# Kernel tuning notes

Hardware: AMD Instinct MI355X
Metric: run time of the kernel (lower is better)

## Reference

```python
import jax, jax.numpy as jnp
import numpy as np

N_NODES = 50000
IN_DIM = 256
LATENT = 128
HIDDEN = 2 * LATENT  # 256


def _xavier(key, fan_in, fan_out):
    # matches nn.init.xavier_uniform_ on a [out, in] weight; we store as [in, out]
    limit = float(np.sqrt(6.0 / (fan_in + fan_out)))
    return jax.random.uniform(key, (fan_in, fan_out), jnp.float32, -limit, limit)


def setup_inputs() -> dict:
    key = jax.random.key(0)
    ks = jax.random.split(key, 8)
    x = jax.random.normal(ks[0], (N_NODES, IN_DIM), jnp.float32)
    edge_index = jax.random.randint(ks[1], (2, 800000), 0, N_NODES, jnp.int64)
    W1 = _xavier(ks[2], IN_DIM, HIDDEN)
    b1 = jnp.zeros((HIDDEN,), jnp.float32)
    Wmu = _xavier(ks[3], HIDDEN, LATENT)
    bmu = jnp.zeros((LATENT,), jnp.float32)
    Wlv = _xavier(ks[4], HIDDEN, LATENT)
    blv = jnp.zeros((LATENT,), jnp.float32)
    return {"x": x, "edge_index": edge_index, "W1": W1, "b1": b1,
            "Wmu": Wmu, "bmu": bmu, "Wlv": Wlv, "blv": blv}


def _gcn_layer(x, W, b, src, dst):
    # PyG GCNConv: h = x @ W; add self loops; symmetric norm; scatter-add; + bias
    h = x @ W  # [N, out]
    ones = jnp.ones(src.shape[0], x.dtype)
    deg = jax.ops.segment_sum(ones, dst, num_segments=N_NODES) + 1.0  # +1 for self loop
    dinv = jax.lax.rsqrt(deg)  # deg >= 1 always
    norm = dinv[src] * dinv[dst]  # [E]
    agg = jax.ops.segment_sum(h[src] * norm[:, None], dst, num_segments=N_NODES)
    agg = agg + h * (dinv * dinv)[:, None]  # self-loop contribution, norm_ii = 1/deg_i
    return agg + b


def reference(x, edge_index, W1, b1, Wmu, bmu, Wlv, blv):
    src, dst = edge_index[0], edge_index[1]
    z = _gcn_layer(x, W1, b1, src, dst)
    z = jax.nn.relu(z)
    # dropout in eval mode == identity
    mu = _gcn_layer(z, Wmu, bmu, src, dst)
    logvar = _gcn_layer(z, Wlv, blv, src, dst)
    return (mu, logvar)
```

## Files before the change

kernel.cpp:

```cpp
#include <hip/hip_runtime.h>

#define N_NODES 50000
#define E_EDGES 800000
#define D 256
#define L 128
#define CAP 64

typedef __attribute__((ext_vector_type(8))) short bf16x8;
typedef __attribute__((ext_vector_type(4))) float f32x4;

__device__ __forceinline__ float bf2f(unsigned short u) {
    union { unsigned int i; float f; } v; v.i = ((unsigned int)u) << 16; return v.f;
}
__device__ __forceinline__ unsigned short f2bf(float f) {
    union { float f; unsigned int i; } v; v.f = f;
    unsigned int r = v.i + 0x7fffu + ((v.i >> 16) & 1u);
    return (unsigned short)(r >> 16);
}

__global__ __launch_bounds__(256) void fill_fixed(const int* __restrict__ src,
                                                  const int* __restrict__ dst,
                                                  int* __restrict__ cursor,
                                                  int* __restrict__ bucket) {
    int e = blockIdx.x * 256 + threadIdx.x;
    if (e >= E_EDGES) return;
    int d = dst[e];
    int pos = atomicAdd(&cursor[d], 1);
    if (pos < CAP) bucket[d * CAP + pos] = src[e];
}

__global__ __launch_bounds__(256) void setup_t(
    const float* __restrict__ W1, const float* __restrict__ Wmu,
    const float* __restrict__ Wlv, const float* __restrict__ bmu,
    const float* __restrict__ blv,
    unsigned short* __restrict__ W1h, unsigned short* __restrict__ W1l,
    unsigned short* __restrict__ Wch,
    float* __restrict__ bcat, int* __restrict__ cursor) {
    int b = blockIdx.x, t = threadIdx.x;
    if (b < 128) {
        __shared__ float tile[32][33];
        int m = b >> 6;
        int ti = b & 63;
        int k0 = (ti >> 3) * 32, n0 = (ti & 7) * 32;
        int rr = t >> 5, cc = t & 31;
#pragma unroll
        for (int p = 0; p < 4; ++p) {
            int kk = p * 8 + rr;
            int k = k0 + kk, n = n0 + cc;
            float w;
            if (m == 0) w = W1[k * 256 + n];
            else        w = (n < 128) ? Wmu[k * 128 + n] : Wlv[k * 128 + (n - 128)];
            tile[kk][cc] = w;
        }
        __syncthreads();
#pragma unroll
        for (int p = 0; p < 4; ++p) {
            int nn = p * 8 + rr;
            float w = tile[cc][nn];
            unsigned short h = f2bf(w);
            int n = n0 + nn, k = k0 + cc;
            if (m == 0) {
                W1h[n * 256 + k] = h;
                W1l[n * 256 + k] = f2bf(w - bf2f(h));
            } else {
                Wch[n * 256 + k] = h;
            }
        }
        if (b == 64) bcat[t] = (t < 128) ? bmu[t] : blv[t - 128];
    } else {
        int i = (b - 128) * 256 + t;
        if (i < N_NODES) cursor[i] = 0;
    }
}

__global__ __launch_bounds__(256, 2) void gemm_mfma(
    const float* __restrict__ A,
    const unsigned short* __restrict__ Bth, const unsigned short* __restrict__ Btl,
    unsigned short* __restrict__ Hout, int M)
{
    __shared__ unsigned short Ash[128 * 32];
    __shared__ unsigned short Asl[128 * 32];
    __shared__ unsigned short Bsh[256 * 32];
    __shared__ unsigned short Bsl[256 * 32];
    const int t = threadIdx.x;
    const int lane = t & 63, wave = t >> 6;
    const int m_ = lane & 15, q = lane >> 4;
    const int wr = wave >> 1, wc = wave & 1;
    const int row0 = blockIdx.x * 128;
    const int sr = t >> 2;
    const int sc = t & 3;

    f32x4 acc[4][8];
    const f32x4 zf = {0.f, 0.f, 0.f, 0.f};
#pragma unroll
    for (int rs = 0; rs < 4; ++rs)
#pragma unroll
        for (int nt = 0; nt < 8; ++nt) acc[rs][nt] = zf;

    for (int ks = 0; ks < 8; ++ks) {
        const int k0 = ks * 32;
        bf16x8 gbh[4], gbl[4];
#pragma unroll
        for (int i = 0; i < 4; ++i) {
            int n = sr + i * 64;
            gbh[i] = *(const bf16x8*)(Bth + n * 256 + k0 + sc * 8);
            gbl[i] = *(const bf16x8*)(Btl + n * 256 + k0 + sc * 8);
        }
        float4 ga0[2], ga1[2];
#pragma unroll
        for (int p = 0; p < 2; ++p) {
            int r = row0 + p * 64 + sr; if (r >= M) r = M - 1;
            const float* Xp = A + (size_t)r * 256 + k0 + sc * 8;
            ga0[p] = *(const float4*)Xp;
            ga1[p] = *(const float4*)(Xp + 4);
        }
        __syncthreads();
#pragma unroll
        for (int p = 0; p < 2; ++p) {
            int lr = p * 64 + sr;
            int cc = (sc ^ ((lr >> 1) & 3)) * 8;
            float af[8] = {ga0[p].x, ga0[p].y, ga0[p].z, ga0[p].w,
                           ga1[p].x, ga1[p].y, ga1[p].z, ga1[p].w};
            bf16x8 h, l;
#pragma unroll
            for (int j = 0; j < 8; ++j) {
                unsigned short hh = f2bf(af[j]);
                h[j] = (short)hh;
                l[j] = (short)f2bf(af[j] - bf2f(hh));
            }
            *(bf16x8*)&Ash[lr * 32 + cc] = h;
            *(bf16x8*)&Asl[lr * 32 + cc] = l;
        }
#pragma unroll
        for (int i = 0; i < 4; ++i) {
            int n = sr + i * 64;
            int cc = (sc ^ ((n >> 1) & 3)) * 8;
            *(bf16x8*)&Bsh[n * 32 + cc] = gbh[i];
            *(bf16x8*)&Bsl[n * 32 + cc] = gbl[i];
        }
        __syncthreads();
        bf16x8 ah[4], al[4];
#pragma unroll
        for (int rs = 0; rs < 4; ++rs) {
            int r = wr * 64 + rs * 16 + m_;
            int cc = (q ^ ((r >> 1) & 3)) * 8;
            ah[rs] = *(const bf16x8*)&Ash[r * 32 + cc];
            al[rs] = *(const bf16x8*)&Asl[r * 32 + cc];
        }
#pragma unroll
        for (int nt = 0; nt < 8; ++nt) {
            int n = wc * 128 + nt * 16 + m_;
            int cr = (q ^ ((n >> 1) & 3)) * 8;
            bf16x8 bh = *(const bf16x8*)&Bsh[n * 32 + cr];
            bf16x8 bl = *(const bf16x8*)&Bsl[n * 32 + cr];
#pragma unroll
            for (int rs = 0; rs < 4; ++rs) {
                acc[rs][nt] = __builtin_amdgcn_mfma_f32_16x16x32_bf16(ah[rs], bh, acc[rs][nt], 0, 0, 0);
                acc[rs][nt] = __builtin_amdgcn_mfma_f32_16x16x32_bf16(ah[rs], bl, acc[rs][nt], 0, 0, 0);
                acc[rs][nt] = __builtin_amdgcn_mfma_f32_16x16x32_bf16(al[rs], bh, acc[rs][nt], 0, 0, 0);
            }
        }
    }
#pragma unroll
    for (int rs = 0; rs < 4; ++rs) {
        int rbase = row0 + wr * 64 + rs * 16 + q * 4;
#pragma unroll
        for (int rr = 0; rr < 4; ++rr) {
            int grow = rbase + rr;
            if (grow >= M) continue;
#pragma unroll
            for (int nt = 0; nt < 8; ++nt) {
                int gcol = wc * 128 + nt * 16 + m_;
                Hout[(size_t)grow * 256 + gcol] = f2bf(acc[rs][nt][rr]);
            }
        }
    }
}

__global__ __launch_bounds__(256, 2) void gemm_bf16(
    const unsigned short* __restrict__ A,
    const unsigned short* __restrict__ Bth,
    unsigned short* __restrict__ Tout, int M)
{
    __shared__ unsigned short Ash[128 * 32];
    __shared__ unsigned short Bsh[256 * 32];
    const int t = threadIdx.x;
    const int lane = t & 63, wave = t >> 6;
    const int m_ = lane & 15, q = lane >> 4;
    const int wr = wave >> 1, wc = wave & 1;
    const int row0 = blockIdx.x * 128;
    const int sr = t >> 2;
    const int sc = t & 3;

    f32x4 acc[4][8];
    const f32x4 zf = {0.f, 0.f, 0.f, 0.f};
#pragma unroll
    for (int rs = 0; rs < 4; ++rs)
#pragma unroll
        for (int nt = 0; nt < 8; ++nt) acc[rs][nt] = zf;

    for (int ks = 0; ks < 8; ++ks) {
        const int k0 = ks * 32;
        bf16x8 gbh[4];
#pragma unroll
        for (int i = 0; i < 4; ++i) {
            int n = sr + i * 64;
            gbh[i] = *(const bf16x8*)(Bth + n * 256 + k0 + sc * 8);
        }
        bf16x8 gav[2];
#pragma unroll
        for (int p = 0; p < 2; ++p) {
            int r = row0 + p * 64 + sr; if (r >= M) r = M - 1;
            gav[p] = *(const bf16x8*)(A + (size_t)r * 256 + k0 + sc * 8);
        }
        __syncthreads();
#pragma unroll
        for (int p = 0; p < 2; ++p) {
            int lr = p * 64 + sr;
            int cc = (sc ^ ((lr >> 1) & 3)) * 8;
            *(bf16x8*)&Ash[lr * 32 + cc] = gav[p];
        }
#pragma unroll
        for (int i = 0; i < 4; ++i) {
            int n = sr + i * 64;
            int cc = (sc ^ ((n >> 1) & 3)) * 8;
            *(bf16x8*)&Bsh[n * 32 + cc] = gbh[i];
        }
        __syncthreads();
        bf16x8 ah[4];
#pragma unroll
        for (int rs = 0; rs < 4; ++rs) {
            int r = wr * 64 + rs * 16 + m_;
            int cc = (q ^ ((r >> 1) & 3)) * 8;
            ah[rs] = *(const bf16x8*)&Ash[r * 32 + cc];
        }
#pragma unroll
        for (int nt = 0; nt < 8; ++nt) {
            int n = wc * 128 + nt * 16 + m_;
            int cr = (q ^ ((n >> 1) & 3)) * 8;
            bf16x8 bh = *(const bf16x8*)&Bsh[n * 32 + cr];
#pragma unroll
            for (int rs = 0; rs < 4; ++rs) {
                acc[rs][nt] = __builtin_amdgcn_mfma_f32_16x16x32_bf16(ah[rs], bh, acc[rs][nt], 0, 0, 0);
            }
        }
    }
#pragma unroll
    for (int rs = 0; rs < 4; ++rs) {
        int rbase = row0 + wr * 64 + rs * 16 + q * 4;
#pragma unroll
        for (int rr = 0; rr < 4; ++rr) {
            int grow = rbase + rr;
            if (grow >= M) continue;
#pragma unroll
            for (int nt = 0; nt < 8; ++nt) {
                int gcol = wc * 128 + nt * 16 + m_;
                Tout[(size_t)grow * 256 + gcol] = f2bf(acc[rs][nt][rr]);
            }
        }
    }
}

__global__ __launch_bounds__(256) void gather_pre(
    const unsigned short* __restrict__ Hs,
    const int* __restrict__ bucket, const int* __restrict__ cnt_,
    const float* __restrict__ bias,
    unsigned short* __restrict__ OutZ,
    float* __restrict__ mu, float* __restrict__ lv, int mode, int node0)
{
    const int lane = threadIdx.x & 63;
    const int hl = lane & 31;
    const int bb = lane & 32;
    const int node = node0 + blockIdx.x * 8 + (threadIdx.x >> 5);
    const int col = hl * 8;
    int raw = cnt_[node];
    float dn = rsqrtf((float)raw + 1.0f);
    int cnt = raw > CAP ? CAP : raw;

    int   s0r = 0, s1r = 0;
    float w0r = 0.f, w1r = 0.f;
    if (hl < cnt) {
        s0r = bucket[node * CAP + hl];
        w0r = rsqrtf((float)cnt_[s0r] + 1.0f) * dn;
    }
    if (hl + 32 < cnt) {
        s1r = bucket[node * CAP + 32 + hl];
        w1r = rsqrtf((float)cnt_[s1r] + 1.0f) * dn;
    }

    float sl = dn * dn;
    bf16x8 hv = *(const bf16x8*)(Hs + (size_t)node * D + col);
    float a[8];
#pragma unroll
    for (int p = 0; p < 8; ++p) a[p] = bf2f((unsigned short)hv[p]) * sl;

    const int cnt0 = cnt < 32 ? cnt : 32;
    int j = 0;
    for (; j + 3 < cnt0; j += 4) {
        int t0 = __shfl(s0r, bb + j,     64), t1 = __shfl(s0r, bb + j + 1, 64);
        int t2 = __shfl(s0r, bb + j + 2, 64), t3 = __shfl(s0r, bb + j + 3, 64);
        float w0 = __shfl(w0r, bb + j,     64), w1 = __shfl(w0r, bb + j + 1, 64);
        float w2 = __shfl(w0r, bb + j + 2, 64), w3 = __shfl(w0r, bb + j + 3, 64);
        bf16x8 u0 = *(const bf16x8*)(Hs + (size_t)t0 * D + col);
        bf16x8 u1 = *(const bf16x8*)(Hs + (size_t)t1 * D + col);
        bf16x8 u2 = *(const bf16x8*)(Hs + (size_t)t2 * D + col);
        bf16x8 u3 = *(const bf16x8*)(Hs + (size_t)t3 * D + col);
#pragma unroll
        for (int p = 0; p < 8; ++p) a[p] = fmaf(bf2f((unsigned short)u0[p]), w0, a[p]);
#pragma unroll
        for (int p = 0; p < 8; ++p) a[p] = fmaf(bf2f((unsigned short)u1[p]), w1, a[p]);
#pragma unroll
        for (int p = 0; p < 8; ++p) a[p] = fmaf(bf2f((unsigned short)u2[p]), w2, a[p]);
#pragma unroll
        for (int p = 0; p < 8; ++p) a[p] = fmaf(bf2f((unsigned short)u3[p]), w3, a[p]);
    }
    for (; j < cnt0; ++j) {
        int   t0 = __shfl(s0r, bb + j, 64);
        float w0 = __shfl(w0r, bb + j, 64);
        bf16x8 u0 = *(const bf16x8*)(Hs + (size_t)t0 * D + col);
#pragma unroll
        for (int p = 0; p < 8; ++p) a[p] = fmaf(bf2f((unsigned short)u0[p]), w0, a[p]);
    }
    if (cnt > 32) {
        for (int j2 = 0; j2 < cnt - 32; ++j2) {
            int   t0 = __shfl(s1r, bb + j2, 64);
            float w0 = __shfl(w1r, bb + j2, 64);
            bf16x8 u0 = *(const bf16x8*)(Hs + (size_t)t0 * D + col);
#pragma unroll
            for (int p = 0; p < 8; ++p) a[p] = fmaf(bf2f((unsigned short)u0[p]), w0, a[p]);
        }
    }

    float4 b0 = *(const float4*)(bias + col);
    float4 b1 = *(const float4*)(bias + col + 4);
    float bf[8] = {b0.x, b0.y, b0.z, b0.w, b1.x, b1.y, b1.z, b1.w};
    if (mode == 0) {
        bf16x8 o;
#pragma unroll
        for (int p = 0; p < 8; ++p) o[p] = (short)f2bf(fmaxf(a[p] + bf[p], 0.f));
        *(bf16x8*)(OutZ + (size_t)node * D + col) = o;
    } else {
        float4 o0, o1;
        o0.x = a[0] + bf[0]; o0.y = a[1] + bf[1];
        o0.z = a[2] + bf[2]; o0.w = a[3] + bf[3];
        o1.x = a[4] + bf[4]; o1.y = a[5] + bf[5];
        o1.z = a[6] + bf[6]; o1.w = a[7] + bf[7];
        float* Op = (col < 128) ? (mu + (size_t)node * L + col)
                                : (lv + (size_t)node * L + (col - 128));
        *(float4*)Op = o0;
        *(float4*)(Op + 4) = o1;
    }
}

extern "C" void kernel_launch(void* const* d_in, const int* in_sizes, int n_in,
                              void* d_out, int out_size, void* d_ws, size_t ws_size,
                              hipStream_t stream) {
    const float* x   = (const float*)d_in[0];
    const int*   ei  = (const int*)d_in[1];
    const float* W1  = (const float*)d_in[2];
    const float* b1  = (const float*)d_in[3];
    const float* Wmu = (const float*)d_in[4];
    const float* bmu = (const float*)d_in[5];
    const float* Wlv = (const float*)d_in[6];
    const float* blv = (const float*)d_in[7];
    const int* src = ei;
    const int* dst = ei + E_EDGES;

    const size_t NF = (size_t)N_NODES * D;
    unsigned short* Hb = (unsigned short*)d_ws;
    unsigned short* Z  = Hb + NF;
    unsigned short* T  = Z + NF;
    unsigned short* W1h = T + NF;
    unsigned short* W1l = W1h + 65536;
    unsigned short* Wch = W1l + 65536;
    unsigned short* Wcl = Wch + 65536;
    float* bcat = (float*)(Wcl + 65536);
    int* cursor = (int*)(bcat + 256);
    int* bucket = cursor + N_NODES;
    float* mu = (float*)d_out;
    float* lv = mu + (size_t)N_NODES * L;

    setup_t<<<128 + (N_NODES + 255) / 256, 256, 0, stream>>>(
        W1, Wmu, Wlv, bmu, blv, W1h, W1l, Wch, bcat, cursor);
    fill_fixed<<<(E_EDGES + 255) / 256, 256, 0, stream>>>(src, dst, cursor, bucket);

    const int gemm_blocks = (N_NODES + 127) / 128;
    const int gat_blocks  = (N_NODES / 2) / 8;
    gemm_mfma<<<gemm_blocks, 256, 0, stream>>>(x, W1h, W1l, Hb, N_NODES);
    gather_pre<<<gat_blocks, 256, 0, stream>>>(Hb, bucket, cursor, b1,
                                               Z, nullptr, nullptr, 0, 0);
    gather_pre<<<gat_blocks, 256, 0, stream>>>(Hb, bucket, cursor, b1,
                                               Z, nullptr, nullptr, 0, N_NODES / 2);
    gemm_bf16<<<gemm_blocks, 256, 0, stream>>>(Z, Wch, T, N_NODES);
    gather_pre<<<gat_blocks, 256, 0, stream>>>(T, bucket, cursor, bcat,
                                               nullptr, mu, lv, 1, 0);
    gather_pre<<<gat_blocks, 256, 0, stream>>>(T, bucket, cursor, bcat,
                                               nullptr, mu, lv, 1, N_NODES / 2);
}
```

Measured before the change: 320.3 us.

## Fuse edge bucketing into first GEMM launch and store bucket indices as 16-bit

The separate edge-bucketing kernel is folded into the first MFMA GEMM launch: of every 9 blocks, one runs a GEMM tile and eight scatter edges into per-destination buckets, so the atomic fill overlaps the GEMM instead of running as its own launch. Bucket entries become unsigned short instead of int, halving bucket write and read traffic in the gather kernels. Node ids reach 49999, which fits in 16 bits. Fill blocks share the 256-thread launch bounds and occupancy limits of the GEMM, and their scattered atomics may contend with GEMM memory traffic.

```diff
diff --git a/kernel.cpp b/kernel.cpp
--- a/kernel.cpp
+++ b/kernel.cpp
@@ -16,17 +16,6 @@
     union { float f; unsigned int i; } v; v.f = f;
     unsigned int r = v.i + 0x7fffu + ((v.i >> 16) & 1u);
     return (unsigned short)(r >> 16);
-}
-
-__global__ __launch_bounds__(256) void fill_fixed(const int* __restrict__ src,
-                                                  const int* __restrict__ dst,
-                                                  int* __restrict__ cursor,
-                                                  int* __restrict__ bucket) {
-    int e = blockIdx.x * 256 + threadIdx.x;
-    if (e >= E_EDGES) return;
-    int d = dst[e];
-    int pos = atomicAdd(&cursor[d], 1);
-    if (pos < CAP) bucket[d * CAP + pos] = src[e];
 }
 
 __global__ __launch_bounds__(256) void setup_t(
@@ -73,20 +62,35 @@
     }
 }
 
-__global__ __launch_bounds__(256, 2) void gemm_mfma(
+__global__ __launch_bounds__(256, 2) void gemm1_fill(
     const float* __restrict__ A,
     const unsigned short* __restrict__ Bth, const unsigned short* __restrict__ Btl,
-    unsigned short* __restrict__ Hout, int M)
+    unsigned short* __restrict__ Hout, int M,
+    const int* __restrict__ src, const int* __restrict__ dst,
+    int* __restrict__ cursor, unsigned short* __restrict__ bucket)
 {
     __shared__ unsigned short Ash[128 * 32];
     __shared__ unsigned short Asl[128 * 32];
     __shared__ unsigned short Bsh[256 * 32];
     __shared__ unsigned short Bsl[256 * 32];
+    const int bid = blockIdx.x;
+    const int qb = bid / 9, rb = bid - qb * 9;
     const int t = threadIdx.x;
+
+    if (rb != 0) {
+        int e = (bid - qb - 1) * 256 + t;
+        if (e < E_EDGES) {
+            int d = dst[e];
+            int pos = atomicAdd(&cursor[d], 1);
+            if (pos < CAP) bucket[d * CAP + pos] = (unsigned short)src[e];
+        }
+        return;
+    }
+
     const int lane = t & 63, wave = t >> 6;
     const int m_ = lane & 15, q = lane >> 4;
     const int wr = wave >> 1, wc = wave & 1;
-    const int row0 = blockIdx.x * 128;
+    const int row0 = qb * 128;
     const int sr = t >> 2;
     const int sc = t & 3;
 
@@ -263,7 +267,7 @@
 
 __global__ __launch_bounds__(256) void gather_pre(
     const unsigned short* __restrict__ Hs,
-    const int* __restrict__ bucket, const int* __restrict__ cnt_,
+    const unsigned short* __restrict__ bucket, const int* __restrict__ cnt_,
     const float* __restrict__ bias,
     unsigned short* __restrict__ OutZ,
     float* __restrict__ mu, float* __restrict__ lv, int mode, int node0)
@@ -280,11 +284,11 @@
     int   s0r = 0, s1r = 0;
     float w0r = 0.f, w1r = 0.f;
     if (hl < cnt) {
-        s0r = bucket[node * CAP + hl];
+        s0r = (int)bucket[node * CAP + hl];
         w0r = rsqrtf((float)cnt_[s0r] + 1.0f) * dn;
     }
     if (hl + 32 < cnt) {
-        s1r = bucket[node * CAP + 32 + hl];
+        s1r = (int)bucket[node * CAP + 32 + hl];
         w1r = rsqrtf((float)cnt_[s1r] + 1.0f) * dn;
     }
 
@@ -373,20 +377,20 @@
     unsigned short* W1h = T + NF;
     unsigned short* W1l = W1h + 65536;
     unsigned short* Wch = W1l + 65536;
-    unsigned short* Wcl = Wch + 65536;
-    float* bcat = (float*)(Wcl + 65536);
+    unsigned short* bucket = Wch + 65536;
+    float* bcat = (float*)(bucket + (size_t)N_NODES * CAP);
     int* cursor = (int*)(bcat + 256);
-    int* bucket = cursor + N_NODES;
     float* mu = (float*)d_out;
     float* lv = mu + (size_t)N_NODES * L;
 
     setup_t<<<128 + (N_NODES + 255) / 256, 256, 0, stream>>>(
         W1, Wmu, Wlv, bmu, blv, W1h, W1l, Wch, bcat, cursor);
-    fill_fixed<<<(E_EDGES + 255) / 256, 256, 0, stream>>>(src, dst, cursor, bucket);
+
+    gemm1_fill<<<3516, 256, 0, stream>>>(x, W1h, W1l, Hb, N_NODES,
+                                         src, dst, cursor, bucket);
 
     const int gemm_blocks = (N_NODES + 127) / 128;
     const int gat_blocks  = (N_NODES / 2) / 8;
-    gemm_mfma<<<gemm_blocks, 256, 0, stream>>>(x, W1h, W1l, Hb, N_NODES);
     gather_pre<<<gat_blocks, 256, 0, stream>>>(Hb, bucket, cursor, b1,
                                                Z, nullptr, nullptr, 0, 0);
     gather_pre<<<gat_blocks, 256, 0, stream>>>(Hb, bucket, cursor, b1,
```

Result: faster. 313.5 us (-2.1%).
